# Kernel tuning notes

Measured on AMD Instinct MI355X. Metric: run time of the kernel, lower is better.

## Reference

```python
import jax, jax.numpy as jnp
import numpy as np

RES = 0.005
PRIMES = jnp.array([1, 2654435761, 805459861], dtype=jnp.uint32)
# x-fastest corner order to match w = wx[[0,1,0,1,0,1,0,1]] * wy[[0,0,1,1,0,0,1,1]] * wz[[0,0,0,0,1,1,1,1]]
CORNERS = jnp.array([[0,0,0],[1,0,0],[0,1,0],[1,1,0],[0,0,1],[1,0,1],[0,1,1],[1,1,1]], dtype=jnp.int32)


def setup_inputs() -> dict:
    key = jax.random.key(0)
    k1, k2 = jax.random.split(key)
    N, buckets, d = 2_000_000, 4_194_304, 8
    pts = jax.random.uniform(k1, (N, 3), dtype=jnp.float32)  # points in [0,1)^3
    voxel_features = jax.random.normal(k2, (buckets, d), dtype=jnp.float32) * 0.01
    return {"pts": pts, "voxel_features": voxel_features}


def reference(pts, voxel_features):
    buckets = voxel_features.shape[0]
    q = pts / RES                                   # (N,3) continuous grid coords
    base = jnp.floor(q).astype(jnp.int32)           # (N,3)
    idx = base[:, None, :] + CORNERS[None, :, :]    # (N,8,3) corner voxel indices
    # Instant-NGP spatial hash: xor of coordinate*prime products, mod table size
    hp = idx.astype(jnp.uint32) * PRIMES            # (N,8,3), uint32 wraparound
    slot = ((hp[..., 0] ^ hp[..., 1] ^ hp[..., 2]) % jnp.uint32(buckets)).astype(jnp.int32)
    feat = voxel_features[slot]                     # (N,8,d) gather
    # trilinear weights: prod over axes of frac (corner=1) or 1-frac (corner=0)
    frac = q - base.astype(q.dtype)                 # (N,3)
    c = CORNERS.astype(q.dtype)                     # (8,3)
    w = jnp.prod(jnp.where(c[None, :, :] > 0, frac[:, None, :], 1.0 - frac[:, None, :]), axis=-1)  # (N,8)
    return jnp.einsum('nk,nkd->nd', w, feat)        # (N,d)
```

## Files before the change

kernel.cpp:

```cpp
#include <hip/hip_runtime.h>


__global__ __launch_bounds__(256) void ngp_hash_interp2(
    const float* __restrict__ pts,
    const float4* __restrict__ feat4,
    float4* __restrict__ out4,
    int N, unsigned buckets, int is_pow2)
{
    int t = blockIdx.x * blockDim.x + threadIdx.x;
    int i = t >> 1;
    unsigned h = (unsigned)(t & 1);
    if (i >= N) return;

    float px = pts[3 * i + 0];
    float py = pts[3 * i + 1];
    float pz = pts[3 * i + 2];

    float qx = px / 0.005f;
    float qy = py / 0.005f;
    float qz = pz / 0.005f;

    float bx = floorf(qx), by = floorf(qy), bz = floorf(qz);
    float fx = qx - bx, fy = qy - by, fz = qz - bz;

    unsigned ux = (unsigned)(int)bx;
    unsigned uy = (unsigned)(int)by;
    unsigned uz = (unsigned)(int)bz;

    unsigned hx0 = ux;
    unsigned hx1 = ux + 1u;
    unsigned hy0 = uy * 2654435761u;
    unsigned hy1 = (uy + 1u) * 2654435761u;
    unsigned hz0 = uz * 805459861u;
    unsigned hz1 = (uz + 1u) * 805459861u;

    unsigned hsh[8] = {
        hx0 ^ hy0 ^ hz0,
        hx1 ^ hy0 ^ hz0,
        hx0 ^ hy1 ^ hz0,
        hx1 ^ hy1 ^ hz0,
        hx0 ^ hy0 ^ hz1,
        hx1 ^ hy0 ^ hz1,
        hx0 ^ hy1 ^ hz1,
        hx1 ^ hy1 ^ hz1,
    };

    unsigned off[8];
    if (is_pow2) {
        unsigned mask = buckets - 1u;
        #pragma unroll
        for (int c = 0; c < 8; ++c) off[c] = (hsh[c] & mask) * 2u + h;
    } else {
        #pragma unroll
        for (int c = 0; c < 8; ++c) off[c] = (hsh[c] % buckets) * 2u + h;
    }

    float4 f[8];
    #pragma unroll
    for (int c = 0; c < 8; ++c) f[c] = feat4[off[c]];

    float wx0 = 1.0f - fx, wx1 = fx;
    float wy0 = 1.0f - fy, wy1 = fy;
    float wz0 = 1.0f - fz, wz1 = fz;
    float w[8] = {
        (wx0 * wy0) * wz0, (wx1 * wy0) * wz0,
        (wx0 * wy1) * wz0, (wx1 * wy1) * wz0,
        (wx0 * wy0) * wz1, (wx1 * wy0) * wz1,
        (wx0 * wy1) * wz1, (wx1 * wy1) * wz1,
    };

    float4 a = make_float4(0.f, 0.f, 0.f, 0.f);
    #pragma unroll
    for (int c = 0; c < 8; ++c) {
        a.x += w[c] * f[c].x;
        a.y += w[c] * f[c].y;
        a.z += w[c] * f[c].z;
        a.w += w[c] * f[c].w;
    }

    out4[(size_t)i * 2u + h] = a;
}

extern "C" void kernel_launch(void* const* d_in, const int* in_sizes, int n_in,
                              void* d_out, int out_size, void* d_ws, size_t ws_size,
                              hipStream_t stream) {
    const float* pts  = (const float*)d_in[0];
    const float4* feat4 = (const float4*)d_in[1];
    float4* out4 = (float4*)d_out;

    int N = in_sizes[0] / 3;
    unsigned buckets = (unsigned)(in_sizes[1] / 8);
    int is_pow2 = ((buckets & (buckets - 1u)) == 0u) ? 1 : 0;

    const int block = 256;
    const long long total = 2LL * N;
    const int grid = (int)((total + block - 1) / block);
    hipLaunchKernelGGL(ngp_hash_interp2, dim3(grid), dim3(block), 0, stream,
                       pts, feat4, out4, N, buckets, is_pow2);
}
```

Measured before the change: 193.3 us.

## Sort points by Morton tile bins before hashed trilinear gather

```diff
diff --git a/kernel.cpp b/kernel.cpp
--- a/kernel.cpp
+++ b/kernel.cpp
@@ -1,25 +1,115 @@
 #include <hip/hip_runtime.h>
 
 
-__global__ __launch_bounds__(256) void ngp_hash_interp2(
-    const float* __restrict__ pts,
+#define TILE_SHIFT 2
+#define MBITS 6
+#define NBINS (1u << (3 * MBITS))
+#define SCAN_BLOCK 256
+#define NPARTIALS (NBINS / SCAN_BLOCK)
+
+__device__ __forceinline__ unsigned part1by2(unsigned x) {
+    x &= 0x3Fu;
+    x = (x | (x << 16)) & 0x030000FFu;
+    x = (x | (x << 8))  & 0x0300F00Fu;
+    x = (x | (x << 4))  & 0x030C30C3u;
+    x = (x | (x << 2))  & 0x09249249u;
+    return x;
+}
+
+__device__ __forceinline__ unsigned point_bin(float px, float py, float pz) {
+    float qx = px / 0.005f, qy = py / 0.005f, qz = pz / 0.005f;
+    int cx = (int)floorf(qx), cy = (int)floorf(qy), cz = (int)floorf(qz);
+    unsigned tx = ((unsigned)cx) >> TILE_SHIFT;
+    unsigned ty = ((unsigned)cy) >> TILE_SHIFT;
+    unsigned tz = ((unsigned)cz) >> TILE_SHIFT;
+    return part1by2(tx) | (part1by2(ty) << 1) | (part1by2(tz) << 2);
+}
+
+__global__ __launch_bounds__(256) void hist_kernel(
+    const float* __restrict__ pts, unsigned* __restrict__ bins, int N)
+{
+    int i = blockIdx.x * blockDim.x + threadIdx.x;
+    if (i >= N) return;
+    unsigned b = point_bin(pts[3*i], pts[3*i+1], pts[3*i+2]);
+    atomicAdd(&bins[b], 1u);
+}
+
+__global__ __launch_bounds__(SCAN_BLOCK) void scan_blocks_kernel(
+    unsigned* __restrict__ bins, unsigned* __restrict__ partials)
+{
+    __shared__ unsigned s[SCAN_BLOCK];
+    int t = threadIdx.x;
+    int g = blockIdx.x * SCAN_BLOCK + t;
+    unsigned v = bins[g];
+    s[t] = v;
+    __syncthreads();
+    #pragma unroll
+    for (int d = 1; d < SCAN_BLOCK; d <<= 1) {
+        unsigned add = (t >= d) ? s[t - d] : 0u;
+        __syncthreads();
+        s[t] += add;
+        __syncthreads();
+    }
+    bins[g] = s[t] - v;
+    if (t == SCAN_BLOCK - 1) partials[blockIdx.x] = s[t];
+}
+
+__global__ __launch_bounds__(SCAN_BLOCK) void scan_partials_kernel(
+    unsigned* __restrict__ partials)
+{
+    __shared__ unsigned s[SCAN_BLOCK];
+    int t = threadIdx.x;
+    unsigned v[4], sum = 0u;
+    #pragma unroll
+    for (int j = 0; j < 4; ++j) { v[j] = partials[4*t + j]; sum += v[j]; }
+    s[t] = sum;
+    __syncthreads();
+    #pragma unroll
+    for (int d = 1; d < SCAN_BLOCK; d <<= 1) {
+        unsigned add = (t >= d) ? s[t - d] : 0u;
+        __syncthreads();
+        s[t] += add;
+        __syncthreads();
+    }
+    unsigned run = s[t] - sum;
+    #pragma unroll
+    for (int j = 0; j < 4; ++j) { partials[4*t + j] = run; run += v[j]; }
+}
+
+__global__ __launch_bounds__(256) void scatter_kernel(
+    const float* __restrict__ pts, unsigned* __restrict__ bins,
+    const unsigned* __restrict__ partials, float4* __restrict__ sorted, int N)
+{
+    int i = blockIdx.x * blockDim.x + threadIdx.x;
+    if (i >= N) return;
+    float px = pts[3*i], py = pts[3*i+1], pz = pts[3*i+2];
+    unsigned b = point_bin(px, py, pz);
+    unsigned pos = partials[b >> 8] + atomicAdd(&bins[b], 1u);
+    float4 e; e.x = px; e.y = py; e.z = pz; e.w = __uint_as_float((unsigned)i);
+    sorted[pos] = e;
+}
+
+__global__ __launch_bounds__(256) void ngp_hash_interp_sorted(
+    const float4* __restrict__ sorted,
     const float4* __restrict__ feat4,
     float4* __restrict__ out4,
-    int N, unsigned buckets, int is_pow2)
-{
-    int t = blockIdx.x * blockDim.x + threadIdx.x;
+    int N, unsigned buckets, int is_pow2, int nwg)
+{
+    int orig = blockIdx.x;
+    int q = nwg >> 3, r = nwg & 7;
+    int xcd = orig & 7, lq = orig >> 3;
+    int bid = (xcd < r ? xcd * (q + 1) : r * (q + 1) + (xcd - r) * q) + lq;
+
+    int t = bid * 256 + (int)threadIdx.x;
     int i = t >> 1;
     unsigned h = (unsigned)(t & 1);
     if (i >= N) return;
 
-    float px = pts[3 * i + 0];
-    float py = pts[3 * i + 1];
-    float pz = pts[3 * i + 2];
-
-    float qx = px / 0.005f;
-    float qy = py / 0.005f;
-    float qz = pz / 0.005f;
-
+    float4 e = sorted[i];
+    float px = e.x, py = e.y, pz = e.z;
+    unsigned oidx = __float_as_uint(e.w);
+
+    float qx = px / 0.005f, qy = py / 0.005f, qz = pz / 0.005f;
     float bx = floorf(qx), by = floorf(qy), bz = floorf(qz);
     float fx = qx - bx, fy = qy - by, fz = qz - bz;
 
@@ -27,22 +117,15 @@
     unsigned uy = (unsigned)(int)by;
     unsigned uz = (unsigned)(int)bz;
 
-    unsigned hx0 = ux;
-    unsigned hx1 = ux + 1u;
-    unsigned hy0 = uy * 2654435761u;
-    unsigned hy1 = (uy + 1u) * 2654435761u;
-    unsigned hz0 = uz * 805459861u;
-    unsigned hz1 = (uz + 1u) * 805459861u;
+    unsigned hx0 = ux, hx1 = ux + 1u;
+    unsigned hy0 = uy * 2654435761u, hy1 = (uy + 1u) * 2654435761u;
+    unsigned hz0 = uz * 805459861u,  hz1 = (uz + 1u) * 805459861u;
 
     unsigned hsh[8] = {
-        hx0 ^ hy0 ^ hz0,
-        hx1 ^ hy0 ^ hz0,
-        hx0 ^ hy1 ^ hz0,
-        hx1 ^ hy1 ^ hz0,
-        hx0 ^ hy0 ^ hz1,
-        hx1 ^ hy0 ^ hz1,
-        hx0 ^ hy1 ^ hz1,
-        hx1 ^ hy1 ^ hz1,
+        hx0 ^ hy0 ^ hz0, hx1 ^ hy0 ^ hz0,
+        hx0 ^ hy1 ^ hz0, hx1 ^ hy1 ^ hz0,
+        hx0 ^ hy0 ^ hz1, hx1 ^ hy0 ^ hz1,
+        hx0 ^ hy1 ^ hz1, hx1 ^ hy1 ^ hz1,
     };
 
     unsigned off[8];
@@ -78,13 +161,70 @@
         a.w += w[c] * f[c].w;
     }
 
+    out4[(size_t)oidx * 2u + h] = a;
+}
+
+__global__ __launch_bounds__(256) void ngp_hash_interp2(
+    const float* __restrict__ pts,
+    const float4* __restrict__ feat4,
+    float4* __restrict__ out4,
+    int N, unsigned buckets, int is_pow2)
+{
+    int t = blockIdx.x * blockDim.x + threadIdx.x;
+    int i = t >> 1;
+    unsigned h = (unsigned)(t & 1);
+    if (i >= N) return;
+
+    float px = pts[3*i], py = pts[3*i+1], pz = pts[3*i+2];
+    float qx = px / 0.005f, qy = py / 0.005f, qz = pz / 0.005f;
+    float bx = floorf(qx), by = floorf(qy), bz = floorf(qz);
+    float fx = qx - bx, fy = qy - by, fz = qz - bz;
+    unsigned ux = (unsigned)(int)bx, uy = (unsigned)(int)by, uz = (unsigned)(int)bz;
+    unsigned hx0 = ux, hx1 = ux + 1u;
+    unsigned hy0 = uy * 2654435761u, hy1 = (uy + 1u) * 2654435761u;
+    unsigned hz0 = uz * 805459861u,  hz1 = (uz + 1u) * 805459861u;
+    unsigned hsh[8] = {
+        hx0 ^ hy0 ^ hz0, hx1 ^ hy0 ^ hz0,
+        hx0 ^ hy1 ^ hz0, hx1 ^ hy1 ^ hz0,
+        hx0 ^ hy0 ^ hz1, hx1 ^ hy0 ^ hz1,
+        hx0 ^ hy1 ^ hz1, hx1 ^ hy1 ^ hz1,
+    };
+    unsigned off[8];
+    if (is_pow2) {
+        unsigned mask = buckets - 1u;
+        #pragma unroll
+        for (int c = 0; c < 8; ++c) off[c] = (hsh[c] & mask) * 2u + h;
+    } else {
+        #pragma unroll
+        for (int c = 0; c < 8; ++c) off[c] = (hsh[c] % buckets) * 2u + h;
+    }
+    float4 f[8];
+    #pragma unroll
+    for (int c = 0; c < 8; ++c) f[c] = feat4[off[c]];
+    float wx0 = 1.0f - fx, wx1 = fx;
+    float wy0 = 1.0f - fy, wy1 = fy;
+    float wz0 = 1.0f - fz, wz1 = fz;
+    float w[8] = {
+        (wx0 * wy0) * wz0, (wx1 * wy0) * wz0,
+        (wx0 * wy1) * wz0, (wx1 * wy1) * wz0,
+        (wx0 * wy0) * wz1, (wx1 * wy0) * wz1,
+        (wx0 * wy1) * wz1, (wx1 * wy1) * wz1,
+    };
+    float4 a = make_float4(0.f, 0.f, 0.f, 0.f);
+    #pragma unroll
+    for (int c = 0; c < 8; ++c) {
+        a.x += w[c] * f[c].x;
+        a.y += w[c] * f[c].y;
+        a.z += w[c] * f[c].z;
+        a.w += w[c] * f[c].w;
+    }
     out4[(size_t)i * 2u + h] = a;
 }
 
 extern "C" void kernel_launch(void* const* d_in, const int* in_sizes, int n_in,
                               void* d_out, int out_size, void* d_ws, size_t ws_size,
                               hipStream_t stream) {
-    const float* pts  = (const float*)d_in[0];
+    const float* pts   = (const float*)d_in[0];
     const float4* feat4 = (const float4*)d_in[1];
     float4* out4 = (float4*)d_out;
 
@@ -92,9 +232,35 @@
     unsigned buckets = (unsigned)(in_sizes[1] / 8);
     int is_pow2 = ((buckets & (buckets - 1u)) == 0u) ? 1 : 0;
 
+    size_t need = (size_t)N * 16 + (size_t)NBINS * 4 + (size_t)NPARTIALS * 4;
+    if (ws_size < need) {
+        const int block = 256;
+        const long long total = 2LL * N;
+        const int grid = (int)((total + block - 1) / block);
+        hipLaunchKernelGGL(ngp_hash_interp2, dim3(grid), dim3(block), 0, stream,
+                           pts, feat4, out4, N, buckets, is_pow2);
+        return;
+    }
+
+    float4* sorted = (float4*)d_ws;
+    unsigned* bins = (unsigned*)((char*)d_ws + (size_t)N * 16);
+    unsigned* partials = bins + NBINS;
+
+    hipMemsetAsync(bins, 0, (size_t)NBINS * 4, stream);
+
     const int block = 256;
-    const long long total = 2LL * N;
-    const int grid = (int)((total + block - 1) / block);
-    hipLaunchKernelGGL(ngp_hash_interp2, dim3(grid), dim3(block), 0, stream,
-                       pts, feat4, out4, N, buckets, is_pow2);
-}
+    int gridN = (N + block - 1) / block;
+    hipLaunchKernelGGL(hist_kernel, dim3(gridN), dim3(block), 0, stream,
+                       pts, bins, N);
+    hipLaunchKernelGGL(scan_blocks_kernel, dim3(NBINS / SCAN_BLOCK), dim3(SCAN_BLOCK),
+                       0, stream, bins, partials);
+    hipLaunchKernelGGL(scan_partials_kernel, dim3(1), dim3(SCAN_BLOCK), 0, stream,
+                       partials);
+    hipLaunchKernelGGL(scatter_kernel, dim3(gridN), dim3(block), 0, stream,
+                       pts, bins, partials, sorted, N);
+
+    long long total = 2LL * N;
+    int nwg = (int)((total + block - 1) / block);
+    hipLaunchKernelGGL(ngp_hash_interp_sorted, dim3(nwg), dim3(block), 0, stream,
+                       sorted, feat4, out4, N, buckets, is_pow2, nwg);
+}
```

Result: slower. 349.2 us (+80.7%).

## Bin points into Morton-ordered spatial tiles before hash-grid interpolation

Applied to the files above, without the earlier changes.

```diff
diff --git a/kernel.cpp b/kernel.cpp
--- a/kernel.cpp
+++ b/kernel.cpp
@@ -1,50 +1,52 @@
 #include <hip/hip_runtime.h>
 
 
-__global__ __launch_bounds__(256) void ngp_hash_interp2(
-    const float* __restrict__ pts,
-    const float4* __restrict__ feat4,
-    float4* __restrict__ out4,
-    int N, unsigned buckets, int is_pow2)
+#define TILE_SHIFT 3
+#define MDIM 32
+#define NBINS (MDIM * MDIM * MDIM)
+#define CAP 192
+#define MAIN_BLOCK 384
+
+__device__ __forceinline__ unsigned part1by2(unsigned x) {
+    x &= 0x3Fu;
+    x = (x | (x << 16)) & 0x030000FFu;
+    x = (x | (x << 8))  & 0x0300F00Fu;
+    x = (x | (x << 4))  & 0x030C30C3u;
+    x = (x | (x << 2))  & 0x09249249u;
+    return x;
+}
+
+__device__ __forceinline__ unsigned point_bin(float px, float py, float pz) {
+    float qx = px / 0.005f, qy = py / 0.005f, qz = pz / 0.005f;
+    int cx = (int)floorf(qx), cy = (int)floorf(qy), cz = (int)floorf(qz);
+    unsigned tx = ((unsigned)cx) >> TILE_SHIFT;
+    unsigned ty = ((unsigned)cy) >> TILE_SHIFT;
+    unsigned tz = ((unsigned)cz) >> TILE_SHIFT;
+    tx = min(tx, (unsigned)(MDIM - 1));
+    ty = min(ty, (unsigned)(MDIM - 1));
+    tz = min(tz, (unsigned)(MDIM - 1));
+    return part1by2(tx) | (part1by2(ty) << 1) | (part1by2(tz) << 2);
+}
+
+__device__ __forceinline__ void interp_point(
+    int i, unsigned h, const float* __restrict__ pts,
+    const float4* __restrict__ feat4, float4* __restrict__ out4,
+    unsigned buckets, int is_pow2)
 {
-    int t = blockIdx.x * blockDim.x + threadIdx.x;
-    int i = t >> 1;
-    unsigned h = (unsigned)(t & 1);
-    if (i >= N) return;
-
-    float px = pts[3 * i + 0];
-    float py = pts[3 * i + 1];
-    float pz = pts[3 * i + 2];
-
-    float qx = px / 0.005f;
-    float qy = py / 0.005f;
-    float qz = pz / 0.005f;
-
+    float px = pts[3*i], py = pts[3*i+1], pz = pts[3*i+2];
+    float qx = px / 0.005f, qy = py / 0.005f, qz = pz / 0.005f;
     float bx = floorf(qx), by = floorf(qy), bz = floorf(qz);
     float fx = qx - bx, fy = qy - by, fz = qz - bz;
-
-    unsigned ux = (unsigned)(int)bx;
-    unsigned uy = (unsigned)(int)by;
-    unsigned uz = (unsigned)(int)bz;
-
-    unsigned hx0 = ux;
-    unsigned hx1 = ux + 1u;
-    unsigned hy0 = uy * 2654435761u;
-    unsigned hy1 = (uy + 1u) * 2654435761u;
-    unsigned hz0 = uz * 805459861u;
-    unsigned hz1 = (uz + 1u) * 805459861u;
-
+    unsigned ux = (unsigned)(int)bx, uy = (unsigned)(int)by, uz = (unsigned)(int)bz;
+    unsigned hx0 = ux, hx1 = ux + 1u;
+    unsigned hy0 = uy * 2654435761u, hy1 = (uy + 1u) * 2654435761u;
+    unsigned hz0 = uz * 805459861u,  hz1 = (uz + 1u) * 805459861u;
     unsigned hsh[8] = {
-        hx0 ^ hy0 ^ hz0,
-        hx1 ^ hy0 ^ hz0,
-        hx0 ^ hy1 ^ hz0,
-        hx1 ^ hy1 ^ hz0,
-        hx0 ^ hy0 ^ hz1,
-        hx1 ^ hy0 ^ hz1,
-        hx0 ^ hy1 ^ hz1,
-        hx1 ^ hy1 ^ hz1,
+        hx0 ^ hy0 ^ hz0, hx1 ^ hy0 ^ hz0,
+        hx0 ^ hy1 ^ hz0, hx1 ^ hy1 ^ hz0,
+        hx0 ^ hy0 ^ hz1, hx1 ^ hy0 ^ hz1,
+        hx0 ^ hy1 ^ hz1, hx1 ^ hy1 ^ hz1,
     };
-
     unsigned off[8];
     if (is_pow2) {
         unsigned mask = buckets - 1u;
@@ -54,11 +56,9 @@
         #pragma unroll
         for (int c = 0; c < 8; ++c) off[c] = (hsh[c] % buckets) * 2u + h;
     }
-
     float4 f[8];
     #pragma unroll
     for (int c = 0; c < 8; ++c) f[c] = feat4[off[c]];
-
     float wx0 = 1.0f - fx, wx1 = fx;
     float wy0 = 1.0f - fy, wy1 = fy;
     float wz0 = 1.0f - fz, wz1 = fz;
@@ -68,7 +68,6 @@
         (wx0 * wy0) * wz1, (wx1 * wy0) * wz1,
         (wx0 * wy1) * wz1, (wx1 * wy1) * wz1,
     };
-
     float4 a = make_float4(0.f, 0.f, 0.f, 0.f);
     #pragma unroll
     for (int c = 0; c < 8; ++c) {
@@ -77,14 +76,72 @@
         a.z += w[c] * f[c].z;
         a.w += w[c] * f[c].w;
     }
+    out4[(size_t)i * 2u + h] = a;
+}
 
-    out4[(size_t)i * 2u + h] = a;
+__global__ __launch_bounds__(256) void scatter_bin_kernel(
+    const float* __restrict__ pts, unsigned* __restrict__ count,
+    unsigned* __restrict__ ocount, unsigned* __restrict__ slots,
+    unsigned* __restrict__ ovf, int N)
+{
+    int i = blockIdx.x * blockDim.x + threadIdx.x;
+    if (i >= N) return;
+    unsigned b = point_bin(pts[3*i], pts[3*i+1], pts[3*i+2]);
+    unsigned pos = atomicAdd(&count[b], 1u);
+    if (pos < CAP) {
+        slots[b * CAP + pos] = (unsigned)i;
+    } else {
+        unsigned o = atomicAdd(ocount, 1u);
+        ovf[o] = (unsigned)i;
+    }
+}
+
+__global__ __launch_bounds__(MAIN_BLOCK) void main_sorted_kernel(
+    const float* __restrict__ pts, const unsigned* __restrict__ count,
+    const unsigned* __restrict__ slots, const float4* __restrict__ feat4,
+    float4* __restrict__ out4, unsigned buckets, int is_pow2)
+{
+    int orig = blockIdx.x;
+    int bin = (orig & 7) * (NBINS / 8) + (orig >> 3);
+
+    unsigned cnt = count[bin];
+    cnt = min(cnt, (unsigned)CAP);
+    unsigned s = threadIdx.x >> 1;
+    unsigned h = threadIdx.x & 1;
+    if (s >= cnt) return;
+    int i = (int)slots[bin * CAP + s];
+    interp_point(i, h, pts, feat4, out4, buckets, is_pow2);
+}
+
+__global__ __launch_bounds__(256) void overflow_kernel(
+    const float* __restrict__ pts, const unsigned* __restrict__ ocount,
+    const unsigned* __restrict__ ovf, const float4* __restrict__ feat4,
+    float4* __restrict__ out4, unsigned buckets, int is_pow2)
+{
+    unsigned oc = *ocount;
+    unsigned total = oc * 2u;
+    unsigned stride = gridDim.x * blockDim.x;
+    for (unsigned t = blockIdx.x * blockDim.x + threadIdx.x; t < total; t += stride) {
+        int i = (int)ovf[t >> 1];
+        interp_point(i, t & 1u, pts, feat4, out4, buckets, is_pow2);
+    }
+}
+
+__global__ __launch_bounds__(256) void ngp_hash_interp2(
+    const float* __restrict__ pts, const float4* __restrict__ feat4,
+    float4* __restrict__ out4, int N, unsigned buckets, int is_pow2)
+{
+    int t = blockIdx.x * blockDim.x + threadIdx.x;
+    int i = t >> 1;
+    unsigned h = (unsigned)(t & 1);
+    if (i >= N) return;
+    interp_point(i, h, pts, feat4, out4, buckets, is_pow2);
 }
 
 extern "C" void kernel_launch(void* const* d_in, const int* in_sizes, int n_in,
                               void* d_out, int out_size, void* d_ws, size_t ws_size,
                               hipStream_t stream) {
-    const float* pts  = (const float*)d_in[0];
+    const float* pts    = (const float*)d_in[0];
     const float4* feat4 = (const float4*)d_in[1];
     float4* out4 = (float4*)d_out;
 
@@ -92,9 +149,35 @@
     unsigned buckets = (unsigned)(in_sizes[1] / 8);
     int is_pow2 = ((buckets & (buckets - 1u)) == 0u) ? 1 : 0;
 
+    const size_t off_count = 0;
+    const size_t off_oc    = (size_t)NBINS * 4;
+    const size_t off_slots = off_oc + 256;
+    const size_t off_ovf   = off_slots + (size_t)NBINS * CAP * 4;
+    const size_t need      = off_ovf + (size_t)N * 4;
+
+    if (ws_size < need || N <= 0) {
+        const int block = 256;
+        const long long total = 2LL * N;
+        const int grid = (int)((total + block - 1) / block);
+        if (grid > 0)
+            hipLaunchKernelGGL(ngp_hash_interp2, dim3(grid), dim3(block), 0, stream,
+                               pts, feat4, out4, N, buckets, is_pow2);
+        return;
+    }
+
+    unsigned* count  = (unsigned*)((char*)d_ws + off_count);
+    unsigned* ocount = (unsigned*)((char*)d_ws + off_oc);
+    unsigned* slots  = (unsigned*)((char*)d_ws + off_slots);
+    unsigned* ovf    = (unsigned*)((char*)d_ws + off_ovf);
+
+    hipMemsetAsync(d_ws, 0, off_oc + 4, stream);
+
     const int block = 256;
-    const long long total = 2LL * N;
-    const int grid = (int)((total + block - 1) / block);
-    hipLaunchKernelGGL(ngp_hash_interp2, dim3(grid), dim3(block), 0, stream,
-                       pts, feat4, out4, N, buckets, is_pow2);
+    int gridN = (N + block - 1) / block;
+    hipLaunchKernelGGL(scatter_bin_kernel, dim3(gridN), dim3(block), 0, stream,
+                       pts, count, ocount, slots, ovf, N);
+    hipLaunchKernelGGL(main_sorted_kernel, dim3(NBINS), dim3(MAIN_BLOCK), 0, stream,
+                       pts, count, slots, feat4, out4, buckets, is_pow2);
+    hipLaunchKernelGGL(overflow_kernel, dim3(512), dim3(256), 0, stream,
+                       pts, ocount, ovf, feat4, out4, buckets, is_pow2);
 }
```

After: 391.8 us. 2.03x slower.
